# Performance work log

Hardware: AMD Instinct MI355X
Metric: run time of the kernel (lower is better)

Reference implementation:

```python
import jax, jax.numpy as jnp
import numpy as np

EPS = 1e-6

def elu_fm(x):
    # elu(x) + 1
    return jax.nn.elu(x) + 1.0

def setup_inputs() -> dict:
    key = jax.random.key(0)
    k1, k2, k3 = jax.random.split(key, 3)
    N, L, H, D = 4, 4096, 16, 64
    queries = jax.random.normal(k1, (N, L, H, D), dtype=jnp.float32)
    keys = jax.random.normal(k2, (N, L, H, D), dtype=jnp.float32)
    values = jax.random.normal(k3, (N, L, H, D), dtype=jnp.float32)
    key_mask = jnp.ones((N, L), dtype=jnp.float32)
    return {"queries": queries, "keys": keys, "values": values, "key_mask": key_mask}

def reference(queries, keys, values, key_mask):
    Q = elu_fm(queries)                                  # [n, l, h, d]
    K = elu_fm(keys) * key_mask[:, :, None, None]        # [n, s, h, d]
    # KV accumulation: outer products of keys and values summed over sequence
    KV = jnp.einsum('nshd,nshm->nhmd', K, values)        # [n, h, m, d]
    # Normalizer: Q . sum_s K
    Z = 1.0 / (jnp.einsum('nlhd,nhd->nlh', Q, K.sum(axis=1)) + EPS)
    V = jnp.einsum('nlhd,nhmd,nlh->nlhm', Q, KV, Z)      # [n, l, h, m]
    return V
```

## Files before the change

### kernel.cpp

```cpp
#include <hip/hip_runtime.h>

#define EPS 1e-6f

typedef __attribute__((ext_vector_type(8))) short short8;
typedef __attribute__((ext_vector_type(16))) float f32x16;

__device__ __forceinline__ float elu1(float x) {
    return x > 0.f ? x + 1.f : __expf(x);
}

__device__ __forceinline__ short f2bf(float x) {
    unsigned u = __float_as_uint(x);
    return (short)((u + 0x7FFFu + ((u >> 16) & 1u)) >> 16);
}

__device__ __forceinline__ void gl16(const float* g, float* l) {
    __builtin_amdgcn_global_load_lds(
        (const __attribute__((address_space(1))) unsigned int*)g,
        (__attribute__((address_space(3))) unsigned int*)l, 16, 0, 0);
}

#define VMCNT(n) asm volatile("s_waitcnt vmcnt(" #n ")" ::: "memory")
#define LGKMCNT0() asm volatile("s_waitcnt lgkmcnt(0)" ::: "memory")

template<int STEPS>
__global__ __launch_bounds__(64) void kv_partial_kernel(
    const float* __restrict__ keys, const float* __restrict__ values,
    const float* __restrict__ mask, float* __restrict__ pkv,
    float* __restrict__ pks)
{
    __shared__ float Kls[3][16][64];
    __shared__ float Vls[3][16][64];
    __shared__ float Mls[STEPS * 16];

    const int nh = blockIdx.x;
    const int n = nh >> 4, h = nh & 15;
    const int chunk = blockIdx.y;
    const int l = threadIdx.x;
    const int half = l >> 5, col = l & 31;

    const int s0 = chunk * STEPS * 16;
    const float* kb = keys   + ((size_t)(n * 4096 + s0) * 16 + h) * 64;
    const float* vb = values + ((size_t)(n * 4096 + s0) * 16 + h) * 64;

    const size_t lanerow = (size_t)(l >> 4) * 1024 + (size_t)(l & 15) * 4;

    if (l < STEPS * 4)
        *(float4*)&Mls[l * 4] = *(const float4*)(mask + n * 4096 + s0 + l * 4);

    f32x16 acc[2][2];
    #pragma unroll
    for (int a = 0; a < 2; ++a)
        #pragma unroll
        for (int b = 0; b < 2; ++b)
            #pragma unroll
            for (int r = 0; r < 16; ++r) acc[a][b][r] = 0.f;

    float ks0 = 0.f, ks1 = 0.f;

#define ISSUE(ST)                                                         \
    { _Pragma("unroll")                                                   \
      for (int q = 0; q < 4; ++q) {                                       \
          const size_t go = (size_t)((ST) * 16 + 4 * q) * 1024 + lanerow; \
          gl16(kb + go, &Kls[(ST) % 3][4 * q][0]);                        \
          gl16(vb + go, &Vls[(ST) % 3][4 * q][0]);                        \
      } }

    ISSUE(0);
    ISSUE(1);
    ISSUE(2);
    LGKMCNT0();

    #pragma unroll
    for (int st = 0; st < STEPS; ++st) {
        if (st + 2 < STEPS)      { VMCNT(16); }
        else if (st + 1 < STEPS) { VMCNT(8); }
        else                     { VMCNT(0); }
        const int p = st % 3;
        short8 ka0, ka1, va0, va1;
        #pragma unroll
        for (int j = 0; j < 8; ++j) {
            const int s = 8 * half + j;
            const float msk = Mls[st * 16 + s];
            const float k0 = elu1(Kls[p][s][col]) * msk;
            const float k1 = elu1(Kls[p][s][col + 32]) * msk;
            ks0 += k0; ks1 += k1;
            ka0[j] = f2bf(k0); ka1[j] = f2bf(k1);
            va0[j] = f2bf(Vls[p][s][col]);
            va1[j] = f2bf(Vls[p][s][col + 32]);
        }
        LGKMCNT0();
        acc[0][0] = __builtin_amdgcn_mfma_f32_32x32x16_bf16(ka0, va0, acc[0][0], 0, 0, 0);
        acc[0][1] = __builtin_amdgcn_mfma_f32_32x32x16_bf16(ka0, va1, acc[0][1], 0, 0, 0);
        acc[1][0] = __builtin_amdgcn_mfma_f32_32x32x16_bf16(ka1, va0, acc[1][0], 0, 0, 0);
        acc[1][1] = __builtin_amdgcn_mfma_f32_32x32x16_bf16(ka1, va1, acc[1][1], 0, 0, 0);
        if (st + 3 < STEPS) ISSUE(st + 3);
    }
#undef ISSUE

    ks0 += __shfl_xor(ks0, 32);
    ks1 += __shfl_xor(ks1, 32);
    pks[((size_t)chunk * 64 + nh) * 64 + l] = half ? ks1 : ks0;

    float* pb = pkv + ((size_t)chunk * 64 + nh) * 4096;
    #pragma unroll
    for (int td = 0; td < 2; ++td)
        #pragma unroll
        for (int tm = 0; tm < 2; ++tm)
            #pragma unroll
            for (int r = 0; r < 16; ++r) {
                const int d = 32 * td + (r & 3) + 8 * (r >> 2) + 4 * half;
                pb[(size_t)d * 64 + 32 * tm + col] = acc[td][tm][r];
            }
}

__global__ __launch_bounds__(256) void kv_reduce_kernel(
    const float* __restrict__ pkv, const float* __restrict__ pks,
    float* __restrict__ kvt, float* __restrict__ ksum, int CH)
{
    const int nh = blockIdx.x;
    const int f4 = blockIdx.y * 256 + threadIdx.x;
    float4 s4 = make_float4(0.f, 0.f, 0.f, 0.f);
    #pragma unroll 4
    for (int c = 0; c < CH; ++c) {
        const float4 v = *(const float4*)(pkv + ((size_t)c * 64 + nh) * 4096 + f4 * 4);
        s4.x += v.x; s4.y += v.y; s4.z += v.z; s4.w += v.w;
    }
    *(float4*)(kvt + (size_t)nh * 4096 + f4 * 4) = s4;

    if (blockIdx.y == 0 && threadIdx.x < 64) {
        float s = 0.f;
        #pragma unroll 4
        for (int c = 0; c < CH; ++c)
            s += pks[((size_t)c * 64 + nh) * 64 + threadIdx.x];
        ksum[nh * 64 + threadIdx.x] = s;
    }
}

__global__ __launch_bounds__(256) void out_kernel(
    const float* __restrict__ queries, const float* __restrict__ kvt,
    const float* __restrict__ ksum, float* __restrict__ out)
{
    __shared__ float Qs[64][68];
    __shared__ float KVs[64][68];
    __shared__ float Ksm[64];

    const int nh = blockIdx.x;
    const int n = nh >> 4, h = nh & 15;
    const int t = threadIdx.x;
    const int l0 = blockIdx.y * 64;

    #pragma unroll
    for (int k = 0; k < 4; ++k) {
        const int idx = t + k * 256;
        *(float4*)&KVs[idx >> 4][(idx & 15) * 4] =
            *(const float4*)(kvt + (size_t)nh * 4096 + idx * 4);
    }
    if (t < 64) Ksm[t] = ksum[nh * 64 + t];

    #pragma unroll
    for (int k = 0; k < 4; ++k) {
        const int idx = t + k * 256;
        const int row = idx >> 4, seg = idx & 15;
        const size_t g = ((size_t)(n * 4096 + l0 + row) * 16 + h) * 64 + seg * 4;
        float4 q4 = *(const float4*)(queries + g);
        q4.x = elu1(q4.x);
        q4.y = elu1(q4.y);
        q4.z = elu1(q4.z);
        q4.w = elu1(q4.w);
        *(float4*)&Qs[row][seg * 4] = q4;
    }
    __syncthreads();

    const int mg = t & 7;
    const int lg = t >> 3;

    float acc[2][8];
    float zacc[2] = {0.f, 0.f};
    #pragma unroll
    for (int i = 0; i < 2; ++i)
        #pragma unroll
        for (int j = 0; j < 8; ++j) acc[i][j] = 0.f;

    #pragma unroll 4
    for (int d0 = 0; d0 < 64; d0 += 4) {
        const float4 km4 = *(const float4*)&Ksm[d0];
        float4 q[2];
        q[0] = *(const float4*)&Qs[lg][d0];
        q[1] = *(const float4*)&Qs[lg + 32][d0];
        #pragma unroll
        for (int i = 0; i < 2; ++i)
            zacc[i] += q[i].x * km4.x + q[i].y * km4.y +
                       q[i].z * km4.z + q[i].w * km4.w;
        #pragma unroll
        for (int r = 0; r < 4; ++r) {
            const float4 kva = *(const float4*)&KVs[d0 + r][mg * 4];
            const float4 kvb = *(const float4*)&KVs[d0 + r][32 + mg * 4];
            #pragma unroll
            for (int i = 0; i < 2; ++i) {
                const float qc = ((const float*)&q[i])[r];
                acc[i][0] = fmaf(qc, kva.x, acc[i][0]);
                acc[i][1] = fmaf(qc, kva.y, acc[i][1]);
                acc[i][2] = fmaf(qc, kva.z, acc[i][2]);
                acc[i][3] = fmaf(qc, kva.w, acc[i][3]);
                acc[i][4] = fmaf(qc, kvb.x, acc[i][4]);
                acc[i][5] = fmaf(qc, kvb.y, acc[i][5]);
                acc[i][6] = fmaf(qc, kvb.z, acc[i][6]);
                acc[i][7] = fmaf(qc, kvb.w, acc[i][7]);
            }
        }
    }

    #pragma unroll
    for (int i = 0; i < 2; ++i) {
        const float z = 1.f / (zacc[i] + EPS);
        const int row = l0 + lg + 32 * i;
        const size_t g = ((size_t)(n * 4096 + row) * 16 + h) * 64;
        float4 o;
        o.x = acc[i][0] * z; o.y = acc[i][1] * z;
        o.z = acc[i][2] * z; o.w = acc[i][3] * z;
        *(float4*)(out + g + mg * 4) = o;
        o.x = acc[i][4] * z; o.y = acc[i][5] * z;
        o.z = acc[i][6] * z; o.w = acc[i][7] * z;
        *(float4*)(out + g + 32 + mg * 4) = o;
    }
}

extern "C" void kernel_launch(void* const* d_in, const int* in_sizes, int n_in,
                              void* d_out, int out_size, void* d_ws, size_t ws_size,
                              hipStream_t stream) {
    const float* queries = (const float*)d_in[0];
    const float* keys    = (const float*)d_in[1];
    const float* values  = (const float*)d_in[2];
    const float* mask    = (const float*)d_in[3];
    float* out = (float*)d_out;

    auto need = [](int CH) {
        return ((size_t)CH * 64 * 4096 + (size_t)CH * 64 * 64 +
                (size_t)64 * 4096 + 64 * 64) * sizeof(float);
    };
    const int CH = (need(32) <= ws_size) ? 32 : 16;

    float* pkv  = (float*)d_ws;
    float* pks  = pkv + (size_t)CH * 64 * 4096;
    float* kvt  = pks + (size_t)CH * 64 * 64;
    float* ksum = kvt + (size_t)64 * 4096;

    if (CH == 32)
        kv_partial_kernel<8><<<dim3(64, 32), 64, 0, stream>>>(keys, values, mask, pkv, pks);
    else
        kv_partial_kernel<16><<<dim3(64, 16), 64, 0, stream>>>(keys, values, mask, pkv, pks);
    kv_reduce_kernel<<<dim3(64, 4), 256, 0, stream>>>(pkv, pks, kvt, ksum, CH);
    out_kernel<<<dim3(64, 64), 256, 0, stream>>>(queries, kvt, ksum, out);
}
```

Measured before the change: 88.98 us.

## Use 4-wave blocks in KV partial kernel with register-prefetched tiles and LDS reduction

The KV partial kernel goes from single-wave blocks with async global-to-LDS triple buffering to 256-thread blocks. The four waves cooperatively load 64-row tiles into registers, apply ELU and the mask once per element, and write to LDS, prefetching the next tile during the MFMA work. Partial accumulators from the four waves are combined through an in-block LDS tree reduction, which halves the number of chunks and so cuts partial-sum traffic into the reduce kernel. The cost is extra barriers and a serialized LDS reduction epilogue, plus less latency hiding than the earlier async pipeline.

```diff
diff --git a/kernel.cpp b/kernel.cpp
--- a/kernel.cpp
+++ b/kernel.cpp
@@ -14,39 +14,32 @@
     return (short)((u + 0x7FFFu + ((u >> 16) & 1u)) >> 16);
 }
 
-__device__ __forceinline__ void gl16(const float* g, float* l) {
-    __builtin_amdgcn_global_load_lds(
-        (const __attribute__((address_space(1))) unsigned int*)g,
-        (__attribute__((address_space(3))) unsigned int*)l, 16, 0, 0);
-}
-
-#define VMCNT(n) asm volatile("s_waitcnt vmcnt(" #n ")" ::: "memory")
 #define LGKMCNT0() asm volatile("s_waitcnt lgkmcnt(0)" ::: "memory")
-
-template<int STEPS>
-__global__ __launch_bounds__(64) void kv_partial_kernel(
+#define BAR() do { LGKMCNT0(); __builtin_amdgcn_s_barrier(); \
+                   asm volatile("" ::: "memory"); } while (0)
+
+template<int ITERS>
+__global__ __launch_bounds__(256, 2) void kv_partial_kernel(
     const float* __restrict__ keys, const float* __restrict__ values,
     const float* __restrict__ mask, float* __restrict__ pkv,
     float* __restrict__ pks)
 {
-    __shared__ float Kls[3][16][64];
-    __shared__ float Vls[3][16][64];
-    __shared__ float Mls[STEPS * 16];
-
-    const int nh = blockIdx.x;
-    const int n = nh >> 4, h = nh & 15;
+    __shared__ float Kls[64][64];
+    __shared__ float Vls[64][64];
+    __shared__ float Mls[ITERS * 64];
+
+    const int nh = blockIdx.x, n = nh >> 4, h = nh & 15;
     const int chunk = blockIdx.y;
-    const int l = threadIdx.x;
+    const int t = threadIdx.x, wv = t >> 6, l = t & 63;
     const int half = l >> 5, col = l & 31;
-
-    const int s0 = chunk * STEPS * 16;
+    const int r0 = t >> 4, c4 = (t & 15) * 4;
+
+    const int s0 = chunk * (ITERS * 64);
     const float* kb = keys   + ((size_t)(n * 4096 + s0) * 16 + h) * 64;
     const float* vb = values + ((size_t)(n * 4096 + s0) * 16 + h) * 64;
 
-    const size_t lanerow = (size_t)(l >> 4) * 1024 + (size_t)(l & 15) * 4;
-
-    if (l < STEPS * 4)
-        *(float4*)&Mls[l * 4] = *(const float4*)(mask + n * 4096 + s0 + l * 4);
+    if (t < ITERS * 16)
+        *(float4*)&Mls[t * 4] = *(const float4*)(mask + n * 4096 + s0 + t * 4);
 
     f32x16 acc[2][2];
     #pragma unroll
@@ -55,63 +48,99 @@
         for (int b = 0; b < 2; ++b)
             #pragma unroll
             for (int r = 0; r < 16; ++r) acc[a][b][r] = 0.f;
-
-    float ks0 = 0.f, ks1 = 0.f;
-
-#define ISSUE(ST)                                                         \
-    { _Pragma("unroll")                                                   \
-      for (int q = 0; q < 4; ++q) {                                       \
-          const size_t go = (size_t)((ST) * 16 + 4 * q) * 1024 + lanerow; \
-          gl16(kb + go, &Kls[(ST) % 3][4 * q][0]);                        \
-          gl16(vb + go, &Vls[(ST) % 3][4 * q][0]);                        \
-      } }
-
-    ISSUE(0);
-    ISSUE(1);
-    ISSUE(2);
-    LGKMCNT0();
-
-    #pragma unroll
-    for (int st = 0; st < STEPS; ++st) {
-        if (st + 2 < STEPS)      { VMCNT(16); }
-        else if (st + 1 < STEPS) { VMCNT(8); }
-        else                     { VMCNT(0); }
-        const int p = st % 3;
+    float4 ks4 = make_float4(0.f, 0.f, 0.f, 0.f);
+
+    float4 kr[4], vr[4];
+    #pragma unroll
+    for (int k = 0; k < 4; ++k) {
+        const size_t go = (size_t)(r0 + 16 * k) * 1024 + c4;
+        kr[k] = *(const float4*)(kb + go);
+        vr[k] = *(const float4*)(vb + go);
+    }
+
+    #pragma unroll
+    for (int it = 0; it < ITERS; ++it) {
+        BAR();
+        #pragma unroll
+        for (int k = 0; k < 4; ++k) {
+            const float msk = Mls[it * 64 + r0 + 16 * k];
+            float4 kk = kr[k];
+            kk.x = elu1(kk.x) * msk; kk.y = elu1(kk.y) * msk;
+            kk.z = elu1(kk.z) * msk; kk.w = elu1(kk.w) * msk;
+            ks4.x += kk.x; ks4.y += kk.y; ks4.z += kk.z; ks4.w += kk.w;
+            *(float4*)&Kls[r0 + 16 * k][c4] = kk;
+            *(float4*)&Vls[r0 + 16 * k][c4] = vr[k];
+        }
+        BAR();
+        if (it + 1 < ITERS) {
+            #pragma unroll
+            for (int k = 0; k < 4; ++k) {
+                const size_t go = (size_t)(r0 + 16 * k + 64 * (it + 1)) * 1024 + c4;
+                kr[k] = *(const float4*)(kb + go);
+                vr[k] = *(const float4*)(vb + go);
+            }
+        }
         short8 ka0, ka1, va0, va1;
         #pragma unroll
         for (int j = 0; j < 8; ++j) {
-            const int s = 8 * half + j;
-            const float msk = Mls[st * 16 + s];
-            const float k0 = elu1(Kls[p][s][col]) * msk;
-            const float k1 = elu1(Kls[p][s][col + 32]) * msk;
-            ks0 += k0; ks1 += k1;
-            ka0[j] = f2bf(k0); ka1[j] = f2bf(k1);
-            va0[j] = f2bf(Vls[p][s][col]);
-            va1[j] = f2bf(Vls[p][s][col + 32]);
-        }
-        LGKMCNT0();
+            const int s = 16 * wv + 8 * half + j;
+            ka0[j] = f2bf(Kls[s][col]);
+            ka1[j] = f2bf(Kls[s][col + 32]);
+            va0[j] = f2bf(Vls[s][col]);
+            va1[j] = f2bf(Vls[s][col + 32]);
+        }
         acc[0][0] = __builtin_amdgcn_mfma_f32_32x32x16_bf16(ka0, va0, acc[0][0], 0, 0, 0);
         acc[0][1] = __builtin_amdgcn_mfma_f32_32x32x16_bf16(ka0, va1, acc[0][1], 0, 0, 0);
         acc[1][0] = __builtin_amdgcn_mfma_f32_32x32x16_bf16(ka1, va0, acc[1][0], 0, 0, 0);
         acc[1][1] = __builtin_amdgcn_mfma_f32_32x32x16_bf16(ka1, va1, acc[1][1], 0, 0, 0);
-        if (st + 3 < STEPS) ISSUE(st + 3);
-    }
-#undef ISSUE
-
-    ks0 += __shfl_xor(ks0, 32);
-    ks1 += __shfl_xor(ks1, 32);
-    pks[((size_t)chunk * 64 + nh) * 64 + l] = half ? ks1 : ks0;
-
-    float* pb = pkv + ((size_t)chunk * 64 + nh) * 4096;
-    #pragma unroll
-    for (int td = 0; td < 2; ++td)
-        #pragma unroll
-        for (int tm = 0; tm < 2; ++tm)
-            #pragma unroll
-            for (int r = 0; r < 16; ++r) {
-                const int d = 32 * td + (r & 3) + 8 * (r >> 2) + 4 * half;
-                pb[(size_t)d * 64 + 32 * tm + col] = acc[td][tm][r];
-            }
+    }
+
+    BAR();
+    *(float4*)&Kls[r0][c4] = ks4;
+    BAR();
+    if (t < 64) {
+        float s = 0.f;
+        #pragma unroll
+        for (int r = 0; r < 16; ++r) s += Kls[r][t];
+        pks[((size_t)chunk * 64 + nh) * 64 + t] = s;
+    }
+    BAR();
+
+    float* cb0 = &Kls[0][0];
+    float* cb1 = &Vls[0][0];
+#define FLATW(BUF)                                                         \
+    { _Pragma("unroll") for (int td = 0; td < 2; ++td)                     \
+      _Pragma("unroll") for (int tm = 0; tm < 2; ++tm)                     \
+      _Pragma("unroll") for (int r = 0; r < 16; ++r)                       \
+          BUF[((td * 2 + tm) * 16 + r) * 64 + l] = acc[td][tm][r]; }
+#define FLATR(BUF)                                                         \
+    { _Pragma("unroll") for (int td = 0; td < 2; ++td)                     \
+      _Pragma("unroll") for (int tm = 0; tm < 2; ++tm)                     \
+      _Pragma("unroll") for (int r = 0; r < 16; ++r)                       \
+          acc[td][tm][r] += BUF[((td * 2 + tm) * 16 + r) * 64 + l]; }
+    if (wv == 2) FLATW(cb0);
+    if (wv == 3) FLATW(cb1);
+    BAR();
+    if (wv == 0) FLATR(cb0);
+    if (wv == 1) FLATR(cb1);
+    BAR();
+    if (wv == 1) FLATW(cb0);
+    BAR();
+    if (wv == 0) {
+        FLATR(cb0);
+        float* pb = pkv + ((size_t)chunk * 64 + nh) * 4096;
+        #pragma unroll
+        for (int td = 0; td < 2; ++td)
+            #pragma unroll
+            for (int tm = 0; tm < 2; ++tm)
+                #pragma unroll
+                for (int r = 0; r < 16; ++r) {
+                    const int d = 32 * td + (r & 3) + 8 * (r >> 2) + 4 * half;
+                    pb[(size_t)d * 64 + 32 * tm + col] = acc[td][tm][r];
+                }
+    }
+#undef FLATW
+#undef FLATR
 }
 
 __global__ __launch_bounds__(256) void kv_reduce_kernel(
@@ -239,17 +268,17 @@
         return ((size_t)CH * 64 * 4096 + (size_t)CH * 64 * 64 +
                 (size_t)64 * 4096 + 64 * 64) * sizeof(float);
     };
-    const int CH = (need(32) <= ws_size) ? 32 : 16;
+    const int CH = (need(16) <= ws_size) ? 16 : 8;
 
     float* pkv  = (float*)d_ws;
     float* pks  = pkv + (size_t)CH * 64 * 4096;
     float* kvt  = pks + (size_t)CH * 64 * 64;
     float* ksum = kvt + (size_t)64 * 4096;
 
-    if (CH == 32)
-        kv_partial_kernel<8><<<dim3(64, 32), 64, 0, stream>>>(keys, values, mask, pkv, pks);
+    if (CH == 16)
+        kv_partial_kernel<4><<<dim3(64, 16), 256, 0, stream>>>(keys, values, mask, pkv, pks);
     else
-        kv_partial_kernel<16><<<dim3(64, 16), 64, 0, stream>>>(keys, values, mask, pkv, pks);
+        kv_partial_kernel<8><<<dim3(64, 8), 256, 0, stream>>>(keys, values, mask, pkv, pks);
     kv_reduce_kernel<<<dim3(64, 4), 256, 0, stream>>>(pkv, pks, kvt, ksum, CH);
     out_kernel<<<dim3(64, 64), 256, 0, stream>>>(queries, kvt, ksum, out);
 }
```

Result: faster. 79.76 us (-10.4%).
